# Performance work log

Measured on AMD Instinct MI355X. Metric: run time of the kernel, lower is better.

Reference implementation:

```python
import jax, jax.numpy as jnp
import numpy as np

N_NODES = 50000
N_EDGES = 800000
H = 256
EDGE_DIM = 3
N_LAYERS = 3
MLP_LAYERS = 3


def setup_inputs() -> dict:
    key = jax.random.key(0)
    ks = jax.random.split(key, 16)
    s = 1.0 / np.sqrt(H)
    inp = {
        'x': jax.random.normal(ks[0], (N_NODES, H), dtype=jnp.float32),
        'edge_index': jax.random.randint(ks[1], (2, N_EDGES), 0, N_NODES, dtype=jnp.int64),
        'edge_attr': jax.random.normal(ks[2], (N_EDGES, EDGE_DIM), dtype=jnp.float32),
        # per-layer edge-attr projection Linear(3 -> H)
        'We': jax.random.normal(ks[3], (N_LAYERS, EDGE_DIM, H), dtype=jnp.float32) / np.sqrt(EDGE_DIM),
        'be': jax.random.normal(ks[4], (N_LAYERS, H), dtype=jnp.float32) * 0.01,
        # per-layer inner mlp: MLP_LAYERS linears of [H, H]
        'Wm': jax.random.normal(ks[5], (N_LAYERS, MLP_LAYERS, H, H), dtype=jnp.float32) * s,
        'bm': jax.random.normal(ks[6], (N_LAYERS, MLP_LAYERS, H), dtype=jnp.float32) * 0.01,
        # final projection head: Linear -> ReLU -> Linear
        'pW1': jax.random.normal(ks[7], (H, H), dtype=jnp.float32) * s,
        'pb1': jax.random.normal(ks[8], (H,), dtype=jnp.float32) * 0.01,
        'pW2': jax.random.normal(ks[9], (H, H), dtype=jnp.float32) * s,
        'pb2': jax.random.normal(ks[10], (H,), dtype=jnp.float32) * 0.01,
    }
    return inp


def _inner_mlp(h, Wl, bl):
    # mlp.forward: linear, relu between layers, no relu after last
    for i in range(MLP_LAYERS):
        h = h @ Wl[i] + bl[i]
        if i < MLP_LAYERS - 1:
            h = jax.nn.relu(h)
    return h


def reference(x, edge_index, edge_attr, We, be, Wm, bm, pW1, pb1, pW2, pb2):
    src = edge_index[0]  # x_j (source / message sender)
    dst = edge_index[1]  # x_i (destination / aggregation target)
    for l in range(N_LAYERS):
        x0 = x
        # GINEConv: msg = ReLU(x_j + lin_edge(edge_attr)); sum-agg at dst; eps=0
        e = edge_attr @ We[l] + be[l]                      # [E, H]
        msg = jax.nn.relu(x[src] + e)                      # [E, H] edge gather
        agg = jax.ops.segment_sum(msg, dst, num_segments=N_NODES)  # scatter-sum
        h = _inner_mlp(x + agg, Wm[l], bm[l])              # (1+eps)*x + agg, eps=0
        x = jax.nn.relu(h) + x0                            # residual in gin.forward
    # proj head: Linear -> ReLU -> Linear
    out = jax.nn.relu(x @ pW1 + pb1) @ pW2 + pb2
    return out
```

## Files before the change

kernel.cpp:

```cpp
#include <hip/hip_runtime.h>

#define NNODES 50000
#define NEDGES 800000
#define HD 256
#define NSB 196
#define BM 64
#define BUFB (BM * 512)

typedef __attribute__((ext_vector_type(8))) short bf16x8;
typedef __attribute__((ext_vector_type(4))) float f32x4;

__device__ __forceinline__ unsigned int f2bf(float f) {
    union { float f; unsigned int u; } v; v.f = f;
    unsigned int u = v.u;
    u += 0x7fffu + ((u >> 16) & 1u);
    return u >> 16;
}
__device__ __forceinline__ float b2f(unsigned short u) {
    union { unsigned int u; float f; } v; v.u = ((unsigned int)u) << 16;
    return v.f;
}

__global__ void zero_int(int* __restrict__ p, int n) {
    int i = blockIdx.x * blockDim.x + threadIdx.x;
    if (i < n) p[i] = 0;
}

__global__ __launch_bounds__(256) void x2bf(const float* __restrict__ x,
                                            unsigned short* __restrict__ xb) {
    int i = blockIdx.x * 256 + threadIdx.x;
    float4 v = reinterpret_cast<const float4*>(x)[i];
    ushort4 o;
    o.x = (unsigned short)f2bf(v.x);
    o.y = (unsigned short)f2bf(v.y);
    o.z = (unsigned short)f2bf(v.z);
    o.w = (unsigned short)f2bf(v.w);
    reinterpret_cast<ushort4*>(xb)[i] = o;
}

__global__ __launch_bounds__(256) void hist_kernel(const int* __restrict__ dst,
                                                   int* __restrict__ deg) {
    int e = blockIdx.x * 256 + threadIdx.x;
    if (e < NEDGES) atomicAdd(&deg[dst[e]], 1);
}

__global__ __launch_bounds__(256) void scan_part(const int* __restrict__ deg,
                                                 int* __restrict__ bsum) {
    __shared__ int red[256];
    int t = threadIdx.x;
    int i = blockIdx.x * 256 + t;
    red[t] = (i < NNODES) ? deg[i] : 0;
    __syncthreads();
    for (int off = 128; off > 0; off >>= 1) {
        if (t < off) red[t] += red[t + off];
        __syncthreads();
    }
    if (t == 0) bsum[blockIdx.x] = red[0];
}

__global__ __launch_bounds__(256) void scan_base(const int* __restrict__ bsum,
                                                 int* __restrict__ bbase) {
    __shared__ int s[256];
    int t = threadIdx.x;
    int v = (t < NSB) ? bsum[t] : 0;
    s[t] = v;
    __syncthreads();
    for (int off = 1; off < 256; off <<= 1) {
        int u = (t >= off) ? s[t - off] : 0;
        __syncthreads();
        s[t] += u;
        __syncthreads();
    }
    if (t < NSB) bbase[t] = s[t] - v;
}

__global__ __launch_bounds__(256) void scan_fin(const int* __restrict__ deg,
                                                const int* __restrict__ bbase,
                                                int* __restrict__ rowptr,
                                                int* __restrict__ cursor) {
    __shared__ int s[256];
    int t = threadIdx.x;
    int i = blockIdx.x * 256 + t;
    int v = (i < NNODES) ? deg[i] : 0;
    s[t] = v;
    __syncthreads();
    for (int off = 1; off < 256; off <<= 1) {
        int u = (t >= off) ? s[t - off] : 0;
        __syncthreads();
        s[t] += u;
        __syncthreads();
    }
    int val = bbase[blockIdx.x] + s[t] - v;
    if (i < NNODES) {
        rowptr[i] = val;
        cursor[i] = val;
    }
    if (i == NNODES) rowptr[i] = val;
}

__global__ __launch_bounds__(256) void fill_csr(const int* __restrict__ src,
                                                const int* __restrict__ dst,
                                                const float* __restrict__ ea,
                                                int* __restrict__ cursor,
                                                int4* __restrict__ epack) {
    int e = blockIdx.x * 256 + threadIdx.x;
    if (e >= NEDGES) return;
    int pos = atomicAdd(&cursor[dst[e]], 1);
    int4 v;
    v.x = src[e];
    v.y = __float_as_int(ea[e * 3 + 0]);
    v.z = __float_as_int(ea[e * 3 + 1]);
    v.w = __float_as_int(ea[e * 3 + 2]);
    epack[pos] = v;
}

__global__ __launch_bounds__(256) void agg_kernel(
    const unsigned short* __restrict__ xb, const int* __restrict__ rowptr,
    const int4* __restrict__ epack, const float* __restrict__ We,
    const float* __restrict__ be, unsigned short* __restrict__ out) {
    const int wave = threadIdx.x >> 6;
    const int lane = threadIdx.x & 63;
    const int n = blockIdx.x * 4 + wave;
    const int c = lane * 4;
    const float4 w0 = *reinterpret_cast<const float4*>(We + c);
    const float4 w1 = *reinterpret_cast<const float4*>(We + HD + c);
    const float4 w2 = *reinterpret_cast<const float4*>(We + 2 * HD + c);
    const float4 bb = *reinterpret_cast<const float4*>(be + c);
    ushort4 xv = *reinterpret_cast<const ushort4*>(xb + (size_t)n * HD + c);
    float4 acc = make_float4(b2f(xv.x), b2f(xv.y), b2f(xv.z), b2f(xv.w));
    const int beg = rowptr[n], end = rowptr[n + 1];

#define EDGE_ACC(E, XS)                                                              \
    {                                                                                \
        float a0 = __int_as_float((E).y);                                            \
        float a1 = __int_as_float((E).z);                                            \
        float a2 = __int_as_float((E).w);                                            \
        acc.x += fmaxf(fmaf(a0, w0.x, fmaf(a1, w1.x, fmaf(a2, w2.x,                  \
                       b2f((XS).x) + bb.x))), 0.f);                                  \
        acc.y += fmaxf(fmaf(a0, w0.y, fmaf(a1, w1.y, fmaf(a2, w2.y,                  \
                       b2f((XS).y) + bb.y))), 0.f);                                  \
        acc.z += fmaxf(fmaf(a0, w0.z, fmaf(a1, w1.z, fmaf(a2, w2.z,                  \
                       b2f((XS).z) + bb.z))), 0.f);                                  \
        acc.w += fmaxf(fmaf(a0, w0.w, fmaf(a1, w1.w, fmaf(a2, w2.w,                  \
                       b2f((XS).w) + bb.w))), 0.f);                                  \
    }

    int i = beg;
    for (; i + 4 <= end; i += 4) {
        int4 e0 = epack[i];
        int4 e1 = epack[i + 1];
        int4 e2 = epack[i + 2];
        int4 e3 = epack[i + 3];
        ushort4 s0 = *reinterpret_cast<const ushort4*>(xb + (size_t)e0.x * HD + c);
        ushort4 s1 = *reinterpret_cast<const ushort4*>(xb + (size_t)e1.x * HD + c);
        ushort4 s2 = *reinterpret_cast<const ushort4*>(xb + (size_t)e2.x * HD + c);
        ushort4 s3 = *reinterpret_cast<const ushort4*>(xb + (size_t)e3.x * HD + c);
        EDGE_ACC(e0, s0);
        EDGE_ACC(e1, s1);
        EDGE_ACC(e2, s2);
        EDGE_ACC(e3, s3);
    }
    for (; i < end; ++i) {
        int4 e0 = epack[i];
        ushort4 s0 = *reinterpret_cast<const ushort4*>(xb + (size_t)e0.x * HD + c);
        EDGE_ACC(e0, s0);
    }
#undef EDGE_ACC

    ushort4 o;
    o.x = (unsigned short)f2bf(acc.x);
    o.y = (unsigned short)f2bf(acc.y);
    o.z = (unsigned short)f2bf(acc.z);
    o.w = (unsigned short)f2bf(acc.w);
    *reinterpret_cast<ushort4*>(out + (size_t)n * HD + c) = o;
}

__global__ void pack_w(const float* __restrict__ Wm, const float* __restrict__ pW1,
                       const float* __restrict__ pW2, unsigned short* __restrict__ Wpk) {
    int g = blockIdx.x * 256 + threadIdx.x;
    int mat = g >> 16;
    int r = g & 65535;
    int j = r & 7, lane = (r >> 3) & 63, kb = (r >> 9) & 7, ct = r >> 12;
    int k = kb * 32 + ((lane >> 4) << 3) + j;
    int c = ct * 16 + (lane & 15);
    const float* s = (mat < 9) ? (Wm + (size_t)mat * 65536)
                               : ((mat == 9) ? pW1 : pW2);
    Wpk[g] = (unsigned short)f2bf(s[k * 256 + c]);
}

__device__ __forceinline__ void load_b(const unsigned short* __restrict__ Wp,
                                       int wave, int lane, int kb, bf16x8* dst) {
#pragma unroll
    for (int ct = 0; ct < 2; ++ct)
        dst[ct] = *reinterpret_cast<const bf16x8*>(
            Wp + ((size_t)(((wave * 2 + ct) * 8 + kb) * 64 + lane)) * 8);
}

template <int NPH, bool RELU_LAST, bool RES, bool OUTF32>
__global__ __launch_bounds__(512, 4) void gemm_fused(
    const unsigned short* __restrict__ A, const unsigned short* __restrict__ Wpk,
    const float* __restrict__ b0, const float* __restrict__ b1,
    const float* __restrict__ b2, const unsigned short* __restrict__ res,
    void* __restrict__ outv) {
    __shared__ __align__(16) unsigned char lds[2 * BUFB];
    const int tid = threadIdx.x;
    const int rbase = blockIdx.x * BM;
    const int wave = tid >> 6;
    const int lane = tid & 63;
    const int lr = lane & 15;
    const int lg = lane >> 4;

    bf16x8 bb[3][2];
    load_b(Wpk, wave, lane, 0, bb[0]);
    load_b(Wpk, wave, lane, 1, bb[1]);

    {
        const unsigned char* Ab = (const unsigned char*)A;
#pragma unroll
        for (int it = 0; it < 4; ++it) {
            int r0 = wave * 8 + it * 2;
            int row = r0 + (lane >> 5);
            int cb = (lane & 31) * 16;
            int grow = rbase + row;
            if (grow >= NNODES) grow = NNODES - 1;
            const unsigned char* src =
                Ab + (size_t)grow * 512 + (cb ^ ((row & 7) << 4));
            __builtin_amdgcn_global_load_lds(
                (const __attribute__((address_space(1))) void*)src,
                (__attribute__((address_space(3))) void*)(lds + r0 * 512), 16, 0, 0);
        }
    }
    __syncthreads();

#pragma unroll
    for (int ph = 0; ph < NPH; ++ph) {
        const unsigned short* Wp = Wpk + (size_t)ph * 65536;
        const float* bias = (ph == 0) ? b0 : ((ph == 1) ? b1 : b2);
        unsigned char* rbuf = lds + (ph & 1) * BUFB;
        unsigned char* wbuf = lds + ((ph & 1) ^ 1) * BUFB;

        f32x4 acc[4][2];
#pragma unroll
        for (int rt = 0; rt < 4; ++rt)
#pragma unroll
            for (int ct = 0; ct < 2; ++ct) acc[rt][ct] = (f32x4){0.f, 0.f, 0.f, 0.f};

#pragma unroll
        for (int kb = 0; kb < 8; ++kb) {
            if (kb + 2 < 8) load_b(Wp, wave, lane, kb + 2, bb[(kb + 2) % 3]);
            const int kbyte = kb * 64 + lg * 16;
#pragma unroll
            for (int rt = 0; rt < 4; ++rt) {
                int row = rt * 16 + lr;
                int off = row * 512 + (kbyte ^ ((row & 7) << 4));
                bf16x8 a = *reinterpret_cast<const bf16x8*>(rbuf + off);
#pragma unroll
                for (int ct = 0; ct < 2; ++ct)
                    acc[rt][ct] = __builtin_amdgcn_mfma_f32_16x16x32_bf16(
                        a, bb[kb % 3][ct], acc[rt][ct], 0, 0, 0);
            }
        }

        if (ph < NPH - 1) {
#pragma unroll
            for (int rt = 0; rt < 4; ++rt) {
#pragma unroll
                for (int ct = 0; ct < 2; ++ct) {
                    int c = wave * 32 + ct * 16 + lr;
                    float bv = bias[c];
#pragma unroll
                    for (int i = 0; i < 4; ++i) {
                        int row = rt * 16 + lg * 4 + i;
                        float v = fmaxf(acc[rt][ct][i] + bv, 0.f);
                        int off = row * 512 + ((2 * c) ^ ((row & 7) << 4));
                        *reinterpret_cast<unsigned short*>(wbuf + off) =
                            (unsigned short)f2bf(v);
                    }
                }
            }
            const unsigned short* Wn = Wpk + (size_t)(ph + 1) * 65536;
            load_b(Wn, wave, lane, 0, bb[0]);
            load_b(Wn, wave, lane, 1, bb[1]);
            __syncthreads();
        } else {
#pragma unroll
            for (int rt = 0; rt < 4; ++rt) {
                int row0 = rbase + rt * 16 + lg * 4;
#pragma unroll
                for (int ct = 0; ct < 2; ++ct) {
                    int c = wave * 32 + ct * 16 + lr;
                    float bv = bias[c];
#pragma unroll
                    for (int i = 0; i < 4; ++i) {
                        int row = row0 + i;
                        if (row < NNODES) {
                            float v = acc[rt][ct][i] + bv;
                            if (RELU_LAST) v = fmaxf(v, 0.f);
                            if (RES) v += b2f(res[(size_t)row * HD + c]);
                            if (OUTF32)
                                reinterpret_cast<float*>(outv)[(size_t)row * HD + c] = v;
                            else
                                reinterpret_cast<unsigned short*>(
                                    outv)[(size_t)row * HD + c] =
                                    (unsigned short)f2bf(v);
                        }
                    }
                }
            }
        }
    }
}

extern "C" void kernel_launch(void* const* d_in, const int* in_sizes, int n_in,
                              void* d_out, int out_size, void* d_ws, size_t ws_size,
                              hipStream_t stream) {
    const float* x   = (const float*)d_in[0];
    const int*   ei  = (const int*)d_in[1];
    const float* ea  = (const float*)d_in[2];
    const float* We  = (const float*)d_in[3];
    const float* be  = (const float*)d_in[4];
    const float* Wm  = (const float*)d_in[5];
    const float* bm  = (const float*)d_in[6];
    const float* pW1 = (const float*)d_in[7];
    const float* pb1 = (const float*)d_in[8];
    const float* pW2 = (const float*)d_in[9];
    const float* pb2 = (const float*)d_in[10];
    float* out = (float*)d_out;

    const size_t NH = (size_t)NNODES * HD;
    unsigned short* xb   = (unsigned short*)d_ws;
    unsigned short* curb = xb + NH;
    unsigned short* aggb = curb + NH;
    unsigned short* Wpk  = aggb + NH;
    int* rowptr = (int*)(Wpk + 11 * 65536);
    int* cursor = rowptr + 50004;
    int* deg    = cursor + 50004;
    int* bsum   = deg + 50004;
    int* bbase  = bsum + 256;
    int4* epack = (int4*)d_out;

    const int* srcI = ei;
    const int* dstI = ei + NEDGES;

    x2bf<<<dim3(NH / 4 / 256), dim3(256), 0, stream>>>(x, xb);
    zero_int<<<dim3((NNODES + 255) / 256), dim3(256), 0, stream>>>(deg, NNODES);
    pack_w<<<dim3(11 * 65536 / 256), dim3(256), 0, stream>>>(Wm, pW1, pW2, Wpk);
    hist_kernel<<<dim3((NEDGES + 255) / 256), dim3(256), 0, stream>>>(dstI, deg);
    scan_part<<<dim3(NSB), dim3(256), 0, stream>>>(deg, bsum);
    scan_base<<<dim3(1), dim3(256), 0, stream>>>(bsum, bbase);
    scan_fin<<<dim3(NSB), dim3(256), 0, stream>>>(deg, bbase, rowptr, cursor);
    fill_csr<<<dim3((NEDGES + 255) / 256), dim3(256), 0, stream>>>(srcI, dstI, ea,
                                                                   cursor, epack);

    const int gemm_grid = (NNODES + BM - 1) / BM;
    for (int l = 0; l < 3; ++l) {
        const unsigned short* xin = (l == 0) ? xb : curb;
        agg_kernel<<<dim3(NNODES / 4), dim3(256), 0, stream>>>(
            xin, rowptr, epack, We + (size_t)l * 3 * HD, be + (size_t)l * HD, aggb);
        gemm_fused<3, true, true, false><<<dim3(gemm_grid), dim3(512), 0, stream>>>(
            aggb, Wpk + (size_t)l * 3 * 65536, bm + (size_t)(l * 3 + 0) * HD,
            bm + (size_t)(l * 3 + 1) * HD, bm + (size_t)(l * 3 + 2) * HD, xin, curb);
    }
    gemm_fused<2, false, false, true><<<dim3(gemm_grid), dim3(512), 0, stream>>>(
        curb, Wpk + (size_t)9 * 65536, pb1, pb2, nullptr, nullptr, out);
}
```

Before: 464.3 us.

## Fuse last GIN layer MLP with projection head and merge prep kernels

The final layer's three-linear MLP, its residual and the two-linear projection head now run in one five-phase GEMM kernel. The residual is added inside the intermediate phase epilogue, so the bf16 node features no longer make a round trip through global memory and one launch is dropped. The x-to-bf16 conversion, weight packing and degree zeroing are merged into a single prep kernel. The CSR now stores source indices premultiplied by the hidden size, which removes 64-bit multiplies from the gather. The residual read in the last partial tile can touch rows past the node count, but those addresses fall inside the workspace.

After: 440.7 us. 5.1% less time.

```diff
diff --git a/kernel.cpp b/kernel.cpp
--- a/kernel.cpp
+++ b/kernel.cpp
@@ -21,21 +21,33 @@
     return v.f;
 }
 
-__global__ void zero_int(int* __restrict__ p, int n) {
-    int i = blockIdx.x * blockDim.x + threadIdx.x;
-    if (i < n) p[i] = 0;
-}
-
-__global__ __launch_bounds__(256) void x2bf(const float* __restrict__ x,
-                                            unsigned short* __restrict__ xb) {
+__global__ __launch_bounds__(256) void prep_all(
+    const float* __restrict__ x, unsigned short* __restrict__ xb,
+    const float* __restrict__ Wm, const float* __restrict__ pW1,
+    const float* __restrict__ pW2, unsigned short* __restrict__ Wpk,
+    int* __restrict__ deg) {
     int i = blockIdx.x * 256 + threadIdx.x;
-    float4 v = reinterpret_cast<const float4*>(x)[i];
-    ushort4 o;
-    o.x = (unsigned short)f2bf(v.x);
-    o.y = (unsigned short)f2bf(v.y);
-    o.z = (unsigned short)f2bf(v.z);
-    o.w = (unsigned short)f2bf(v.w);
-    reinterpret_cast<ushort4*>(xb)[i] = o;
+    if (i < 3200000) {
+        float4 v = reinterpret_cast<const float4*>(x)[i];
+        ushort4 o;
+        o.x = (unsigned short)f2bf(v.x);
+        o.y = (unsigned short)f2bf(v.y);
+        o.z = (unsigned short)f2bf(v.z);
+        o.w = (unsigned short)f2bf(v.w);
+        reinterpret_cast<ushort4*>(xb)[i] = o;
+    } else if (i < 3200000 + 11 * 65536) {
+        int g = i - 3200000;
+        int mat = g >> 16;
+        int r = g & 65535;
+        int j = r & 7, lane = (r >> 3) & 63, kb = (r >> 9) & 7, ct = r >> 12;
+        int k = kb * 32 + ((lane >> 4) << 3) + j;
+        int c = ct * 16 + (lane & 15);
+        const float* s = (mat < 9) ? (Wm + (size_t)mat * 65536)
+                                   : ((mat == 9) ? pW1 : pW2);
+        Wpk[g] = (unsigned short)f2bf(s[k * 256 + c]);
+    } else if (i < 3200000 + 11 * 65536 + NNODES) {
+        deg[i - 3200000 - 11 * 65536] = 0;
+    }
 }
 
 __global__ __launch_bounds__(256) void hist_kernel(const int* __restrict__ dst,
@@ -107,7 +119,7 @@
     if (e >= NEDGES) return;
     int pos = atomicAdd(&cursor[dst[e]], 1);
     int4 v;
-    v.x = src[e];
+    v.x = src[e] * HD;
     v.y = __float_as_int(ea[e * 3 + 0]);
     v.z = __float_as_int(ea[e * 3 + 1]);
     v.w = __float_as_int(ea[e * 3 + 2]);
@@ -126,7 +138,8 @@
     const float4 w1 = *reinterpret_cast<const float4*>(We + HD + c);
     const float4 w2 = *reinterpret_cast<const float4*>(We + 2 * HD + c);
     const float4 bb = *reinterpret_cast<const float4*>(be + c);
-    ushort4 xv = *reinterpret_cast<const ushort4*>(xb + (size_t)n * HD + c);
+    const unsigned short* xbc = xb + c;
+    ushort4 xv = *reinterpret_cast<const ushort4*>(xbc + (size_t)n * HD);
     float4 acc = make_float4(b2f(xv.x), b2f(xv.y), b2f(xv.z), b2f(xv.w));
     const int beg = rowptr[n], end = rowptr[n + 1];
 
@@ -151,10 +164,10 @@
         int4 e1 = epack[i + 1];
         int4 e2 = epack[i + 2];
         int4 e3 = epack[i + 3];
-        ushort4 s0 = *reinterpret_cast<const ushort4*>(xb + (size_t)e0.x * HD + c);
-        ushort4 s1 = *reinterpret_cast<const ushort4*>(xb + (size_t)e1.x * HD + c);
-        ushort4 s2 = *reinterpret_cast<const ushort4*>(xb + (size_t)e2.x * HD + c);
-        ushort4 s3 = *reinterpret_cast<const ushort4*>(xb + (size_t)e3.x * HD + c);
+        ushort4 s0 = *reinterpret_cast<const ushort4*>(xbc + e0.x);
+        ushort4 s1 = *reinterpret_cast<const ushort4*>(xbc + e1.x);
+        ushort4 s2 = *reinterpret_cast<const ushort4*>(xbc + e2.x);
+        ushort4 s3 = *reinterpret_cast<const ushort4*>(xbc + e3.x);
         EDGE_ACC(e0, s0);
         EDGE_ACC(e1, s1);
         EDGE_ACC(e2, s2);
@@ -162,7 +175,7 @@
     }
     for (; i < end; ++i) {
         int4 e0 = epack[i];
-        ushort4 s0 = *reinterpret_cast<const ushort4*>(xb + (size_t)e0.x * HD + c);
+        ushort4 s0 = *reinterpret_cast<const ushort4*>(xbc + e0.x);
         EDGE_ACC(e0, s0);
     }
 #undef EDGE_ACC
@@ -175,19 +188,6 @@
     *reinterpret_cast<ushort4*>(out + (size_t)n * HD + c) = o;
 }
 
-__global__ void pack_w(const float* __restrict__ Wm, const float* __restrict__ pW1,
-                       const float* __restrict__ pW2, unsigned short* __restrict__ Wpk) {
-    int g = blockIdx.x * 256 + threadIdx.x;
-    int mat = g >> 16;
-    int r = g & 65535;
-    int j = r & 7, lane = (r >> 3) & 63, kb = (r >> 9) & 7, ct = r >> 12;
-    int k = kb * 32 + ((lane >> 4) << 3) + j;
-    int c = ct * 16 + (lane & 15);
-    const float* s = (mat < 9) ? (Wm + (size_t)mat * 65536)
-                               : ((mat == 9) ? pW1 : pW2);
-    Wpk[g] = (unsigned short)f2bf(s[k * 256 + c]);
-}
-
 __device__ __forceinline__ void load_b(const unsigned short* __restrict__ Wp,
                                        int wave, int lane, int kb, bf16x8* dst) {
 #pragma unroll
@@ -196,11 +196,12 @@
             Wp + ((size_t)(((wave * 2 + ct) * 8 + kb) * 64 + lane)) * 8);
 }
 
-template <int NPH, bool RELU_LAST, bool RES, bool OUTF32>
+template <int NPH, int RES_PH, bool RELU_LAST, bool OUTF32>
 __global__ __launch_bounds__(512, 4) void gemm_fused(
     const unsigned short* __restrict__ A, const unsigned short* __restrict__ Wpk,
     const float* __restrict__ b0, const float* __restrict__ b1,
-    const float* __restrict__ b2, const unsigned short* __restrict__ res,
+    const float* __restrict__ b2, const float* __restrict__ b3,
+    const float* __restrict__ b4, const unsigned short* __restrict__ res,
     void* __restrict__ outv) {
     __shared__ __align__(16) unsigned char lds[2 * BUFB];
     const int tid = threadIdx.x;
@@ -235,7 +236,10 @@
 #pragma unroll
     for (int ph = 0; ph < NPH; ++ph) {
         const unsigned short* Wp = Wpk + (size_t)ph * 65536;
-        const float* bias = (ph == 0) ? b0 : ((ph == 1) ? b1 : b2);
+        const float* bias = (ph == 0) ? b0
+                          : (ph == 1) ? b1
+                          : (ph == 2) ? b2
+                          : (ph == 3) ? b3 : b4;
         unsigned char* rbuf = lds + (ph & 1) * BUFB;
         unsigned char* wbuf = lds + ((ph & 1) ^ 1) * BUFB;
 
@@ -272,6 +276,8 @@
                     for (int i = 0; i < 4; ++i) {
                         int row = rt * 16 + lg * 4 + i;
                         float v = fmaxf(acc[rt][ct][i] + bv, 0.f);
+                        if (ph == RES_PH)
+                            v += b2f(res[(size_t)(rbase + row) * HD + c]);
                         int off = row * 512 + ((2 * c) ^ ((row & 7) << 4));
                         *reinterpret_cast<unsigned short*>(wbuf + off) =
                             (unsigned short)f2bf(v);
@@ -296,7 +302,8 @@
                         if (row < NNODES) {
                             float v = acc[rt][ct][i] + bv;
                             if (RELU_LAST) v = fmaxf(v, 0.f);
-                            if (RES) v += b2f(res[(size_t)row * HD + c]);
+                            if (RES_PH == NPH - 1)
+                                v += b2f(res[(size_t)row * HD + c]);
                             if (OUTF32)
                                 reinterpret_cast<float*>(outv)[(size_t)row * HD + c] = v;
                             else
@@ -342,9 +349,9 @@
     const int* srcI = ei;
     const int* dstI = ei + NEDGES;
 
-    x2bf<<<dim3(NH / 4 / 256), dim3(256), 0, stream>>>(x, xb);
-    zero_int<<<dim3((NNODES + 255) / 256), dim3(256), 0, stream>>>(deg, NNODES);
-    pack_w<<<dim3(11 * 65536 / 256), dim3(256), 0, stream>>>(Wm, pW1, pW2, Wpk);
+    const int prep_threads = 3200000 + 11 * 65536 + NNODES;
+    prep_all<<<dim3((prep_threads + 255) / 256), dim3(256), 0, stream>>>(
+        x, xb, Wm, pW1, pW2, Wpk, deg);
     hist_kernel<<<dim3((NEDGES + 255) / 256), dim3(256), 0, stream>>>(dstI, deg);
     scan_part<<<dim3(NSB), dim3(256), 0, stream>>>(deg, bsum);
     scan_base<<<dim3(1), dim3(256), 0, stream>>>(bsum, bbase);
@@ -353,14 +360,18 @@
                                                                    cursor, epack);
 
     const int gemm_grid = (NNODES + BM - 1) / BM;
-    for (int l = 0; l < 3; ++l) {
+    for (int l = 0; l < 2; ++l) {
         const unsigned short* xin = (l == 0) ? xb : curb;
         agg_kernel<<<dim3(NNODES / 4), dim3(256), 0, stream>>>(
             xin, rowptr, epack, We + (size_t)l * 3 * HD, be + (size_t)l * HD, aggb);
-        gemm_fused<3, true, true, false><<<dim3(gemm_grid), dim3(512), 0, stream>>>(
+        gemm_fused<3, 2, true, false><<<dim3(gemm_grid), dim3(512), 0, stream>>>(
             aggb, Wpk + (size_t)l * 3 * 65536, bm + (size_t)(l * 3 + 0) * HD,
-            bm + (size_t)(l * 3 + 1) * HD, bm + (size_t)(l * 3 + 2) * HD, xin, curb);
-    }
-    gemm_fused<2, false, false, true><<<dim3(gemm_grid), dim3(512), 0, stream>>>(
-        curb, Wpk + (size_t)9 * 65536, pb1, pb2, nullptr, nullptr, out);
-}
+            bm + (size_t)(l * 3 + 1) * HD, bm + (size_t)(l * 3 + 2) * HD,
+            nullptr, nullptr, xin, curb);
+    }
+    agg_kernel<<<dim3(NNODES / 4), dim3(256), 0, stream>>>(
+        curb, rowptr, epack, We + (size_t)2 * 3 * HD, be + (size_t)2 * HD, aggb);
+    gemm_fused<5, 2, false, true><<<dim3(gemm_grid), dim3(512), 0, stream>>>(
+        aggb, Wpk + (size_t)6 * 65536, bm + (size_t)6 * HD, bm + (size_t)7 * HD,
+        bm + (size_t)8 * HD, pb1, pb2, curb, out);
+}
```
